# Kernel optimization log

Measured on AMD Instinct MI355X. Metric: run time of the kernel, lower is better.

The kernel has to match this reference:

```python
import jax, jax.numpy as jnp
from jax import lax
import numpy as np

N_VOX = 50000
B = 2
D, H, W = 8, 160, 160
CIN = 16
G = 3
K = 27
CHANS = [(16, 16), (16, 32), (32, 64), (64, 64), (64, 128)]
NAMES = ['in', 'e1', 'e2', 'e3', 'out']


def setup_inputs() -> dict:
    key = jax.random.key(0)
    ks = jax.random.split(key, 16)
    rng = np.random.default_rng(0)
    # unique active cells -> deterministic scatter/gather rulebook
    lin = rng.choice(B * D * H * W, size=N_VOX, replace=False)
    bz = lin // (D * H * W)
    rem = lin % (D * H * W)
    zz = rem // (H * W)
    yy = (rem % (H * W)) // W
    xx = rem % W
    coors = jnp.asarray(np.stack([bz, zz, yy, xx], 1).astype(np.int32))
    inp = {
        'voxel_features': jax.random.normal(ks[0], (N_VOX, CIN), jnp.float32),
        'coors': coors,
        'batch_size': B,
    }
    i = 1
    for nm, (ci, co) in zip(NAMES, CHANS):
        k1, k2 = jax.random.split(ks[i]); i += 1
        inp['wb_' + nm] = jax.random.normal(k1, (K, ci, co), jnp.float32) * 0.05
        inp['ws_' + nm] = jax.random.normal(k2, (K, ci, G, co), jnp.float32) * 0.05
        inp['gm_' + nm] = jnp.ones((co,), jnp.float32)
        inp['bt_' + nm] = jnp.zeros((co,), jnp.float32)
    return inp


def _kan_block(feat, nbr, wb, ws, gm, bt, centers, inv_h):
    # submanifold KAN conv: gather -> (silu base + RBF spline basis) GEMM -> accumulate
    n = feat.shape[0]
    fp = jnp.concatenate([feat, jnp.zeros((1, feat.shape[1]), feat.dtype)], 0)  # pad row for out-of-grid

    def body(acc, kin):
        idx, wbk, wsk = kin
        x = fp[idx]                                   # [N, Cin] gathered neighbors
        base = jax.nn.silu(x) @ wbk                   # [N, Cout]
        bas = jnp.exp(-jnp.square((x[:, :, None] - centers) * inv_h))  # [N, Cin, G]
        spl = jnp.einsum('ncg,cgo->no', bas, wsk)     # [N, Cout]
        return acc + base + spl, None

    out0 = jnp.zeros((n, wb.shape[-1]), feat.dtype)
    out, _ = lax.scan(jax.checkpoint(body), out0, (nbr, wb, ws))
    # BatchNorm1d (train-mode batch stats) + ReLU
    mu = out.mean(0)
    var = out.var(0)
    out = (out - mu) * lax.rsqrt(var + 1e-3) * gm + bt
    return jax.nn.relu(out)


def _build_rulebook(coors, batch_size, n):
    grid = jnp.full((batch_size, D + 2, H + 2, W + 2), n, jnp.int32)
    grid = grid.at[coors[:, 0], coors[:, 1] + 1, coors[:, 2] + 1, coors[:, 3] + 1].set(
        jnp.arange(n, dtype=jnp.int32))
    offs = [(dz, dy, dx) for dz in (-1, 0, 1) for dy in (-1, 0, 1) for dx in (-1, 0, 1)]
    return jnp.stack([
        grid[coors[:, 0], coors[:, 1] + 1 + dz, coors[:, 2] + 1 + dy, coors[:, 3] + 1 + dx]
        for dz, dy, dx in offs])  # [27, N]


def reference(voxel_features, coors, batch_size,
              wb_in, ws_in, gm_in, bt_in,
              wb_e1, ws_e1, gm_e1, bt_e1,
              wb_e2, ws_e2, gm_e2, bt_e2,
              wb_e3, ws_e3, gm_e3, bt_e3,
              wb_out, ws_out, gm_out, bt_out):
    n = voxel_features.shape[0]
    nbr = _build_rulebook(coors, batch_size, n)
    centers = jnp.linspace(-1.0, 1.0, G)
    inv_h = (G - 1) / 2.0
    x = _kan_block(voxel_features, nbr, wb_in, ws_in, gm_in, bt_in, centers, inv_h)
    x = _kan_block(x, nbr, wb_e1, ws_e1, gm_e1, bt_e1, centers, inv_h)
    x = _kan_block(x, nbr, wb_e2, ws_e2, gm_e2, bt_e2, centers, inv_h)
    x = _kan_block(x, nbr, wb_e3, ws_e3, gm_e3, bt_e3, centers, inv_h)
    x = _kan_block(x, nbr, wb_out, ws_out, gm_out, bt_out, centers, inv_h)
    co = x.shape[1]
    dense = jnp.zeros((batch_size, D, H, W, co), x.dtype)
    dense = dense.at[coors[:, 0], coors[:, 1], coors[:, 2], coors[:, 3]].set(x)
    dense = dense.transpose(0, 4, 1, 2, 3)            # [B, C, D, H, W]
    return dense.reshape(batch_size, co * D, H, W)    # [B, C*D, H, W]
```

## Files before the change

### kernel.cpp

```cpp
#include <hip/hip_runtime.h>

#define N_VOX 50000
#define BATCH 2
#define DD 8
#define HH 160
#define WW 160
#define PD 10
#define PH 162
#define PW 162
#define KK 27
#define NCELL (BATCH*DD*HH*WW)
#define GRID_ELEMS (BATCH*PD*PH*PW)
#define OUT_ELEMS (BATCH*128*DD*HH*WW)

typedef __attribute__((ext_vector_type(8))) short short8v;
typedef __attribute__((ext_vector_type(4))) float float4v;

__device__ inline unsigned short f2bf(float f) {
    unsigned u = __float_as_uint(f);
    u += 0x7FFFu + ((u >> 16) & 1u);
    return (unsigned short)(u >> 16);
}

__device__ inline void gload_lds16(const void* g, void* l) {
    __builtin_amdgcn_global_load_lds(
        (const __attribute__((address_space(1))) void*)g,
        (__attribute__((address_space(3))) void*)l, 16, 0, 0);
}

__global__ void k_flags(const int* __restrict__ coors, int* __restrict__ flags) {
    int n = blockIdx.x * 256 + threadIdx.x;
    if (n >= N_VOX) return;
    int b = coors[n*4+0], z = coors[n*4+1], y = coors[n*4+2], x = coors[n*4+3];
    flags[((b*DD + z)*HH + y)*WW + x] = 1;
}

__global__ void k_scan1(const int* __restrict__ flags, int* __restrict__ scanout,
                        int* __restrict__ bsums) {
    __shared__ int s[256];
    int t = threadIdx.x, blk = blockIdx.x;
    int4 v = ((const int4*)(flags + blk*1024))[t];
    int tsum = v.x + v.y + v.z + v.w;
    s[t] = tsum; __syncthreads();
    for (int off = 1; off < 256; off <<= 1) {
        int x = (t >= off) ? s[t-off] : 0;
        __syncthreads(); s[t] += x; __syncthreads();
    }
    int excl = s[t] - tsum;
    int4 o; o.x = excl; o.y = excl + v.x; o.z = o.y + v.y; o.w = o.z + v.z;
    ((int4*)(scanout + blk*1024))[t] = o;
    if (t == 255) bsums[blk] = s[255];
}

__global__ void k_scan2(int* __restrict__ bsums) {
    __shared__ int s[512];
    int t = threadIdx.x;
    int orig = (t < 400) ? bsums[t] : 0;
    s[t] = orig; __syncthreads();
    for (int off = 1; off < 512; off <<= 1) {
        int x = (t >= off) ? s[t-off] : 0;
        __syncthreads(); s[t] += x; __syncthreads();
    }
    if (t < 400) bsums[t] = s[t] - orig;
}

__global__ void k_pos(const int* __restrict__ coors, const int* __restrict__ scanout,
                      const int* __restrict__ bsums, int* __restrict__ pos_of,
                      int* __restrict__ vox_at) {
    int n = blockIdx.x * 256 + threadIdx.x;
    if (n >= N_VOX) return;
    int b = coors[n*4+0], z = coors[n*4+1], y = coors[n*4+2], x = coors[n*4+3];
    int lin = ((b*DD + z)*HH + y)*WW + x;
    int pos = scanout[lin] + bsums[lin >> 10];
    pos_of[n] = pos;
    vox_at[pos] = n;
}

__global__ void k_gridP(const int* __restrict__ coors, const int* __restrict__ pos_of,
                        int* __restrict__ gridP) {
    int n = blockIdx.x * 256 + threadIdx.x;
    if (n >= N_VOX) return;
    int b = coors[n*4+0], z = coors[n*4+1], y = coors[n*4+2], x = coors[n*4+3];
    gridP[((b*PD + z+1)*PH + (y+1))*PW + (x+1)] = pos_of[n];
}

__global__ void k_nbrP(const int* __restrict__ coors, const int* __restrict__ vox_at,
                       const int* __restrict__ gridP, int* __restrict__ nbrP) {
    int i = blockIdx.x * 256 + threadIdx.x;
    if (i >= N_VOX) return;
    int n = vox_at[i];
    int b = coors[n*4+0], z = coors[n*4+1]+1, y = coors[n*4+2]+1, x = coors[n*4+3]+1;
    int k = 0;
    for (int dz = -1; dz <= 1; ++dz)
        for (int dy = -1; dy <= 1; ++dy)
            for (int dx = -1; dx <= 1; ++dx) {
                int g = gridP[((b*PD + z+dz)*PH + (y+dy))*PW + (x+dx)];
                nbrP[k*N_VOX + i] = (g >= 0) ? g : N_VOX;
                ++k;
            }
}

__global__ void k_phi0(const float* __restrict__ vf, const int* __restrict__ vox_at,
                       unsigned short* __restrict__ phi) {
    int e = blockIdx.x * 256 + threadIdx.x;
    if (e >= (N_VOX + 1) * 16) return;
    int i = e / 16, c = e % 16;
    float x = 0.f;
    if (i < N_VOX) x = vf[(size_t)vox_at[i] * 16 + c];
    float sig = 1.f / (1.f + __expf(-x));
    ushort4 p;
    p.x = f2bf(x * sig);
    p.y = f2bf(__expf(-(x + 1.f) * (x + 1.f)));
    p.z = f2bf(__expf(-x * x));
    p.w = f2bf(__expf(-(x - 1.f) * (x - 1.f)));
    *(ushort4*)&phi[(size_t)e * 4] = p;
}

struct WswzArgs {
    const float* wb[5];
    const float* ws[5];
    unsigned short* dst[5];
};
__global__ void k_wswz_all(WswzArgs a) {
    constexpr int off[6]   = {0, 27648, 82944, 304128, 746496, 1631232};
    constexpr int lgCI4[5] = {6, 6, 7, 8, 8};
    constexpr int lgCO[5]  = {4, 5, 6, 6, 7};
    int e = blockIdx.x * 256 + threadIdx.x;
    if (e >= off[5]) return;
    int L = 0;
    #pragma unroll
    for (int i = 1; i < 5; ++i) L += (e >= off[i]);
    int el = e - off[L];
    int CIN4 = 1 << lgCI4[L], COUT = 1 << lgCO[L], CIN = CIN4 >> 2;
    int j8   = el & 7;
    int rest = el >> 3;
    int o    = rest & (COUT - 1);
    int kb   = rest >> lgCO[L];
    int kabs = kb * 8 + j8;
    int k  = kabs >> lgCI4[L];
    int c4 = kabs & (CIN4 - 1);
    int c = c4 >> 2, jj = c4 & 3;
    float v = (jj == 0) ? a.wb[L][(k * CIN + c) * COUT + o]
                        : a.ws[L][((k * CIN + c) * 3 + (jj - 1)) * COUT + o];
    a.dst[L][el] = f2bf(v);
}

template<int CIN, int COUT, int NSPL>
__global__ __launch_bounds__(64, 2) void k_conv_mfma(
    const unsigned short* __restrict__ phi,
    const int*            __restrict__ nbrP,
    const unsigned short* __restrict__ Wsw,
    float*                __restrict__ pre,
    float*                __restrict__ sums)
{
    constexpr int CIN4   = CIN * 4;
    constexpr int BK     = 64;
    constexpr int SPK    = CIN4 / BK;
    constexpr int NSTAGE = KK * SPK;
    constexpr int COUTH  = COUT / NSPL;
    constexpr int NFW    = COUTH / 16;
    constexpr int WR     = 4;
    constexpr int NMB    = (N_VOX + 63) / 64;
    constexpr int NBLK   = NMB * NSPL;
    constexpr int PERX   = (NBLK + 7) / 8;

    int lb = blockIdx.x;
    int linear = (lb & 7) * PERX + (lb >> 3);
    if (linear >= NBLK) return;
    const int mb = linear / NSPL, h = linear % NSPL;

    const int lane = threadIdx.x & 63;
    const int l15 = lane & 15, q = lane >> 4;
    const int base = mb * 64;
    int vg[WR];
    #pragma unroll
    for (int rs = 0; rs < WR; ++rs) vg[rs] = base + rs * 16 + l15;
    const int ob = h * COUTH;

    const unsigned short* bp = Wsw + (size_t)(q * COUT + ob + l15) * 8;

    int rows[WR], rowsN[WR];
    short8v A0[2][WR], A1[2][WR];
    short8v B0[2][NFW], B1[2][NFW];

    auto loadB = [&](int sp, short8v (&Bb)[2][NFW]) {
        #pragma unroll
        for (int kk = 0; kk < 2; ++kk)
            #pragma unroll
            for (int nf = 0; nf < NFW; ++nf)
                Bb[kk][nf] = *(const short8v*)(bp +
                    ((size_t)(sp * 8 + kk * 4) * COUT + nf * 16) * 8);
    };
    auto loadA = [&](int sp, short8v (&Ab)[2][WR]) {
        if (sp % SPK == 0) {
            #pragma unroll
            for (int rs = 0; rs < WR; ++rs) rows[rs] = rowsN[rs];
        }
        const int c4s = (sp % SPK) * BK;
        #pragma unroll
        for (int rs = 0; rs < WR; ++rs) {
            const unsigned short* p = phi + (size_t)rows[rs] * CIN4 + c4s + q * 8;
            Ab[0][rs] = *(const short8v*)p;
            Ab[1][rs] = *(const short8v*)(p + 32);
        }
        if (sp % SPK == 0) {
            int k2 = sp / SPK + 1;
            if (k2 < KK) {
                #pragma unroll
                for (int rs = 0; rs < WR; ++rs)
                    rowsN[rs] = (vg[rs] < N_VOX) ? nbrP[k2 * N_VOX + vg[rs]] : N_VOX;
            }
        }
    };

    float4v acc[WR][NFW];
    #pragma unroll
    for (int rs = 0; rs < WR; ++rs)
        #pragma unroll
        for (int nf = 0; nf < NFW; ++nf)
            acc[rs][nf] = (float4v){0.f, 0.f, 0.f, 0.f};

    auto domfma = [&](const short8v (&Ab)[2][WR], const short8v (&Bb)[2][NFW]) {
        #pragma unroll
        for (int kk = 0; kk < 2; ++kk)
            #pragma unroll
            for (int nf = 0; nf < NFW; ++nf)
                #pragma unroll
                for (int rs = 0; rs < WR; ++rs)
                    acc[rs][nf] = __builtin_amdgcn_mfma_f32_16x16x32_bf16(
                        Ab[kk][rs], Bb[kk][nf], acc[rs][nf], 0, 0, 0);
    };

    #pragma unroll
    for (int rs = 0; rs < WR; ++rs) {
        rows[rs]  = (vg[rs] < N_VOX) ? nbrP[vg[rs]] : N_VOX;
        rowsN[rs] = (vg[rs] < N_VOX) ? nbrP[N_VOX + vg[rs]] : N_VOX;
    }
    loadB(0, B0);
    #pragma unroll
    for (int rs = 0; rs < WR; ++rs) {
        const unsigned short* p = phi + (size_t)rows[rs] * CIN4 + q * 8;
        A0[0][rs] = *(const short8v*)p;
        A0[1][rs] = *(const short8v*)(p + 32);
    }

    #define SLOT(T, Ac, Bc, An, Bn)                                   \
        if ((T) + 1 < NSTAGE) { loadB((T) + 1, Bn); loadA((T) + 1, An); } \
        __builtin_amdgcn_sched_barrier(0);                            \
        domfma(Ac, Bc);

    int s = 0;
    for (; s + 2 <= NSTAGE; s += 2) {
        SLOT(s + 0, A0, B0, A1, B1)
        SLOT(s + 1, A1, B1, A0, B0)
    }
    if constexpr (NSTAGE % 2 != 0) {
        domfma(A0, B0);
    }
    #undef SLOT

    #pragma unroll
    for (int rs = 0; rs < WR; ++rs)
        #pragma unroll
        for (int nf = 0; nf < NFW; ++nf)
            #pragma unroll
            for (int r = 0; r < 4; ++r) {
                int v = base + rs * 16 + q * 4 + r;
                if (v < N_VOX)
                    pre[(size_t)v * COUT + ob + nf * 16 + l15] = acc[rs][nf][r];
            }

    float* S = sums + (blockIdx.x & 7) * 256;
    #pragma unroll
    for (int nf = 0; nf < NFW; ++nf) {
        float s1 = 0.f, s2 = 0.f;
        #pragma unroll
        for (int rs = 0; rs < WR; ++rs)
            #pragma unroll
            for (int r = 0; r < 4; ++r) {
                int v = base + rs * 16 + q * 4 + r;
                if (v < N_VOX) {
                    float a = acc[rs][nf][r];
                    s1 += a; s2 += a * a;
                }
            }
        s1 += __shfl_xor(s1, 16); s1 += __shfl_xor(s1, 32);
        s2 += __shfl_xor(s2, 16); s2 += __shfl_xor(s2, 32);
        if (q == 0) {
            atomicAdd(&S[ob + nf * 16 + l15], s1);
            atomicAdd(&S[COUT + ob + nf * 16 + l15], s2);
        }
    }
}

template<int CIN, int COUT>
__global__ __launch_bounds__(256, 2) void k_conv_lds(
    const unsigned short* __restrict__ phi,
    const int*            __restrict__ nbrP,
    const unsigned short* __restrict__ Wsw,
    float*                __restrict__ pre,
    float*                __restrict__ sums)
{
    constexpr int CIN4   = CIN * 4;
    constexpr int BK     = 64;
    constexpr int SPK    = CIN4 / BK;
    constexpr int NSTAGE = KK * SPK;
    constexpr int NFW    = COUT / 32;
    constexpr int NMB    = (N_VOX + 127) / 128;
    constexpr int PERX   = (NMB + 7) / 8;
    constexpr int BENT   = 8 * COUT;
    constexpr int NBI    = (BENT / 64) / 4;

    __shared__ short8v lds[2 * 1024 + 2 * BENT];

    int lb = blockIdx.x;
    int mb = (lb & 7) * PERX + (lb >> 3);
    if (mb >= NMB) return;

    const int t = threadIdx.x, lane = t & 63, w = t >> 6;
    const int l15 = lane & 15, q = lane >> 4;
    const int wm = w >> 1, wn = w & 1;
    const int base = mb * 128;
    const int ob = wn * (COUT / 2);

    short8v* ldsA = lds;
    short8v* ldsB = lds + 2048;

    auto nbrR = [&](int k, int j) -> int {
        return (base + j < N_VOX) ? nbrP[k * N_VOX + base + j] : N_VOX;
    };
    int r0 = nbrR(0, lane), r1 = nbrR(0, 64 + lane);
    int rn0 = nbrR(1, lane), rn1 = nbrR(1, 64 + lane);

    auto stage = [&](int spn) {
        const int nb = spn & 1;
        const int cs = (spn % SPK) * BK;
        #pragma unroll
        for (int i = 0; i < 4; ++i) {
            const int m = w * 4 + i;
            const int c = m >> 1, half = m & 1;
            const unsigned short* src =
                phi + (size_t)(half ? r1 : r0) * CIN4 + cs + c * 8;
            gload_lds16(src, ldsA + nb * 1024 + m * 64);
        }
        #pragma unroll
        for (int i = 0; i < NBI; ++i) {
            const int m = w * NBI + i;
            const unsigned short* src =
                Wsw + ((size_t)spn * BENT + m * 64 + lane) * 8;
            gload_lds16(src, ldsB + nb * BENT + m * 64);
        }
    };

    float4v acc[4][NFW];
    #pragma unroll
    for (int rs = 0; rs < 4; ++rs)
        #pragma unroll
        for (int nf = 0; nf < NFW; ++nf)
            acc[rs][nf] = (float4v){0.f, 0.f, 0.f, 0.f};

    stage(0);
    asm volatile("s_waitcnt vmcnt(0)" ::: "memory");
    __builtin_amdgcn_sched_barrier(0);
    __builtin_amdgcn_s_barrier();
    __builtin_amdgcn_sched_barrier(0);

    for (int sp = 0; sp < NSTAGE; ++sp) {
        const int spn = sp + 1;
        if (spn < NSTAGE) {
            if (spn % SPK == 0) {
                r0 = rn0; r1 = rn1;
                int k2 = spn / SPK + 1;
                if (k2 < KK) { rn0 = nbrR(k2, lane); rn1 = nbrR(k2, 64 + lane); }
            }
            stage(spn);
        }
        __builtin_amdgcn_sched_barrier(0);
        const short8v* A = ldsA + (sp & 1) * 1024 + wm * 64 + l15;
        const short8v* B = ldsB + (sp & 1) * BENT + ob + l15;
        short8v af[2][4], bf[2][NFW];
        #pragma unroll
        for (int kk = 0; kk < 2; ++kk) {
            #pragma unroll
            for (int rs = 0; rs < 4; ++rs)
                af[kk][rs] = A[(kk * 4 + q) * 128 + rs * 16];
            #pragma unroll
            for (int nf = 0; nf < NFW; ++nf)
                bf[kk][nf] = B[(kk * 4 + q) * COUT + nf * 16];
        }
        #pragma unroll
        for (int kk = 0; kk < 2; ++kk)
            #pragma unroll
            for (int nf = 0; nf < NFW; ++nf)
                #pragma unroll
                for (int rs = 0; rs < 4; ++rs)
                    acc[rs][nf] = __builtin_amdgcn_mfma_f32_16x16x32_bf16(
                        af[kk][rs], bf[kk][nf], acc[rs][nf], 0, 0, 0);
        if (spn < NSTAGE) {
            asm volatile("s_waitcnt vmcnt(0)" ::: "memory");
            __builtin_amdgcn_sched_barrier(0);
            __builtin_amdgcn_s_barrier();
            __builtin_amdgcn_sched_barrier(0);
        }
    }

    #pragma unroll
    for (int rs = 0; rs < 4; ++rs)
        #pragma unroll
        for (int nf = 0; nf < NFW; ++nf)
            #pragma unroll
            for (int r = 0; r < 4; ++r) {
                int v = base + wm * 64 + rs * 16 + q * 4 + r;
                if (v < N_VOX)
                    pre[(size_t)v * COUT + ob + nf * 16 + l15] = acc[rs][nf][r];
            }

    float* S = sums + (blockIdx.x & 7) * 256;
    #pragma unroll
    for (int nf = 0; nf < NFW; ++nf) {
        float s1 = 0.f, s2 = 0.f;
        #pragma unroll
        for (int rs = 0; rs < 4; ++rs)
            #pragma unroll
            for (int r = 0; r < 4; ++r) {
                int v = base + wm * 64 + rs * 16 + q * 4 + r;
                if (v < N_VOX) {
                    float a = acc[rs][nf][r];
                    s1 += a; s2 += a * a;
                }
            }
        s1 += __shfl_xor(s1, 16); s1 += __shfl_xor(s1, 32);
        s2 += __shfl_xor(s2, 16); s2 += __shfl_xor(s2, 32);
        if (q == 0) {
            atomicAdd(&S[ob + nf * 16 + l15], s1);
            atomicAdd(&S[COUT + ob + nf * 16 + l15], s2);
        }
    }
}

template<int COUT>
__global__ void k_bnapply_phi(const float* __restrict__ pre, const float* __restrict__ sums,
                              const float* __restrict__ gm, const float* __restrict__ bt,
                              unsigned short* __restrict__ phi) {
    __shared__ float sc[COUT], sh[COUT];
    int t = threadIdx.x;
    if (t < COUT) {
        float s1 = 0.f, s2 = 0.f;
        #pragma unroll
        for (int xo = 0; xo < 8; ++xo) {
            s1 += sums[xo * 256 + t];
            s2 += sums[xo * 256 + COUT + t];
        }
        float mu  = s1 * (1.f / N_VOX);
        float var = s2 * (1.f / N_VOX) - mu*mu;
        float s = rsqrtf(var + 1e-3f) * gm[t];
        sc[t] = s;
        sh[t] = bt[t] - mu * s;
    }
    __syncthreads();
    int tot = (N_VOX + 1) * COUT;
    for (int e = blockIdx.x*256 + t; e < tot; e += gridDim.x*256) {
        int i = e / COUT, c = e % COUT;
        float x = 0.f;
        if (i < N_VOX) x = fmaxf(pre[(size_t)i*COUT + c] * sc[c] + sh[c], 0.f);
        float sig = 1.f / (1.f + __expf(-x));
        ushort4 p;
        p.x = f2bf(x * sig);
        p.y = f2bf(__expf(-(x + 1.f) * (x + 1.f)));
        p.z = f2bf(__expf(-x * x));
        p.w = f2bf(__expf(-(x - 1.f) * (x - 1.f)));
        *(ushort4*)&phi[(size_t)e * 4] = p;
    }
}

template<int COUT>
__global__ void k_bnapply_f32(float* __restrict__ pre, const float* __restrict__ sums,
                              const float* __restrict__ gm, const float* __restrict__ bt) {
    __shared__ float sc[COUT], sh[COUT];
    int t = threadIdx.x;
    if (t < COUT) {
        float s1 = 0.f, s2 = 0.f;
        #pragma unroll
        for (int xo = 0; xo < 8; ++xo) {
            s1 += sums[xo * 256 + t];
            s2 += sums[xo * 256 + COUT + t];
        }
        float mu  = s1 * (1.f / N_VOX);
        float var = s2 * (1.f / N_VOX) - mu*mu;
        float s = rsqrtf(var + 1e-3f) * gm[t];
        sc[t] = s;
        sh[t] = bt[t] - mu * s;
    }
    __syncthreads();
    for (int e = blockIdx.x*256 + t; e < N_VOX*COUT; e += gridDim.x*256) {
        int c = e % COUT;
        pre[e] = fmaxf(pre[e] * sc[c] + sh[c], 0.f);
    }
}

__global__ void k_dense(const float* __restrict__ feat, const int* __restrict__ gridP,
                        float* __restrict__ out) {
    int e4 = blockIdx.x*256 + threadIdx.x;
    if (e4 >= OUT_ELEMS/4) return;
    int e = e4 * 4;
    int x  = e % WW;
    int y  = (e / WW) % HH;
    int cz = (e / (WW*HH)) % (128*DD);
    int b  = e / (WW*HH*128*DD);
    int c = cz >> 3, z = cz & 7;
    const int* gp = &gridP[((b*PD + z+1)*PH + (y+1))*PW + (x+1)];
    int g0 = gp[0], g1 = gp[1], g2 = gp[2], g3 = gp[3];
    float4 o;
    o.x = (g0 >= 0) ? feat[(size_t)g0*128 + c] : 0.f;
    o.y = (g1 >= 0) ? feat[(size_t)g1*128 + c] : 0.f;
    o.z = (g2 >= 0) ? feat[(size_t)g2*128 + c] : 0.f;
    o.w = (g3 >= 0) ? feat[(size_t)g3*128 + c] : 0.f;
    *(float4*)&out[e] = o;
}

template<int CIN, int COUT, int NSPL>
static void run_block(const float* gm, const float* bt,
                      const int* nbrP, unsigned short* phi, const unsigned short* Wsw,
                      float* sums, float* pre, bool last, hipStream_t stream) {
    constexpr int NMB  = (N_VOX + 63) / 64;
    constexpr int NBLK = NMB * NSPL;
    constexpr int GRID = ((NBLK + 7) / 8) * 8;
    k_conv_mfma<CIN, COUT, NSPL><<<GRID, 64, 0, stream>>>(phi, nbrP, Wsw, pre, sums);
    if (last) {
        k_bnapply_f32<COUT><<<512, 256, 0, stream>>>(pre, sums, gm, bt);
    } else {
        k_bnapply_phi<COUT><<<512, 256, 0, stream>>>(pre, sums, gm, bt, phi);
    }
}

template<int CIN, int COUT>
static void run_block_lds(const float* gm, const float* bt,
                          const int* nbrP, unsigned short* phi, const unsigned short* Wsw,
                          float* sums, float* pre, bool last, hipStream_t stream) {
    constexpr int NMB  = (N_VOX + 127) / 128;
    constexpr int GRID = ((NMB + 7) / 8) * 8;
    k_conv_lds<CIN, COUT><<<GRID, 256, 0, stream>>>(phi, nbrP, Wsw, pre, sums);
    if (last) {
        k_bnapply_f32<COUT><<<512, 256, 0, stream>>>(pre, sums, gm, bt);
    } else {
        k_bnapply_phi<COUT><<<512, 256, 0, stream>>>(pre, sums, gm, bt, phi);
    }
}

extern "C" void kernel_launch(void* const* d_in, const int* in_sizes, int n_in,
                              void* d_out, int out_size, void* d_ws, size_t ws_size,
                              hipStream_t stream) {
    const float* vf    = (const float*)d_in[0];
    const int*   coors = (const int*)d_in[1];
    const float* wb[5] = {(const float*)d_in[3],  (const float*)d_in[7],
                          (const float*)d_in[11], (const float*)d_in[15],
                          (const float*)d_in[19]};
    const float* wsp[5]= {(const float*)d_in[4],  (const float*)d_in[8],
                          (const float*)d_in[12], (const float*)d_in[16],
                          (const float*)d_in[20]};
    const float* gm[5] = {(const float*)d_in[5],  (const float*)d_in[9],
                          (const float*)d_in[13], (const float*)d_in[17],
                          (const float*)d_in[21]};
    const float* bt[5] = {(const float*)d_in[6],  (const float*)d_in[10],
                          (const float*)d_in[14], (const float*)d_in[18],
                          (const float*)d_in[22]};

    char* p = (char*)d_ws;
    auto alloc = [&](size_t bytes) {
        char* r = p;
        p += (bytes + 255) & ~(size_t)255;
        return r;
    };
    int*            flags   = (int*)           alloc((size_t)NCELL * 4);
    int*            scanout = (int*)           alloc((size_t)NCELL * 4);
    int*            bsums   = (int*)           alloc(512 * 4);
    int*            pos_of  = (int*)           alloc((size_t)N_VOX * 4);
    int*            vox_at  = (int*)           alloc((size_t)N_VOX * 4);
    int*            gridP   = (int*)           alloc((size_t)GRID_ELEMS * 4);
    int*            nbrP    = (int*)           alloc((size_t)KK * N_VOX * 4);
    unsigned short* Wsw0    = (unsigned short*)alloc((size_t)KK * 64  * 16  * 2);
    unsigned short* Wsw1    = (unsigned short*)alloc((size_t)KK * 64  * 32  * 2);
    unsigned short* Wsw2    = (unsigned short*)alloc((size_t)KK * 128 * 64  * 2);
    unsigned short* Wsw3    = (unsigned short*)alloc((size_t)KK * 256 * 64  * 2);
    unsigned short* Wsw4    = (unsigned short*)alloc((size_t)KK * 256 * 128 * 2);
    unsigned short* phi     = (unsigned short*)alloc((size_t)(N_VOX + 1) * 256 * 2);
    float*          sumsAll = (float*)         alloc(5 * 8 * 256 * 4);
    float*          pre     = (float*)         alloc((size_t)N_VOX * 128 * 4);

    hipMemsetAsync(flags, 0, (size_t)NCELL * 4, stream);
    hipMemsetAsync(gridP, 0xFF, (size_t)GRID_ELEMS * 4, stream);
    hipMemsetAsync(sumsAll, 0, 5 * 8 * 256 * 4, stream);

    WswzArgs wa;
    for (int i = 0; i < 5; ++i) { wa.wb[i] = wb[i]; wa.ws[i] = wsp[i]; }
    wa.dst[0] = Wsw0; wa.dst[1] = Wsw1; wa.dst[2] = Wsw2; wa.dst[3] = Wsw3; wa.dst[4] = Wsw4;
    k_wswz_all<<<(1631232 + 255) / 256, 256, 0, stream>>>(wa);

    k_flags<<<(N_VOX+255)/256, 256, 0, stream>>>(coors, flags);
    k_scan1<<<NCELL/1024, 256, 0, stream>>>(flags, scanout, bsums);
    k_scan2<<<1, 512, 0, stream>>>(bsums);
    k_pos  <<<(N_VOX+255)/256, 256, 0, stream>>>(coors, scanout, bsums, pos_of, vox_at);
    k_gridP<<<(N_VOX+255)/256, 256, 0, stream>>>(coors, pos_of, gridP);
    k_nbrP <<<(N_VOX+255)/256, 256, 0, stream>>>(coors, vox_at, gridP, nbrP);
    {
        int n = (N_VOX + 1) * 16;
        k_phi0<<<(n + 255) / 256, 256, 0, stream>>>(vf, vox_at, phi);
    }

    run_block<16, 16, 1>(gm[0], bt[0], nbrP, phi, Wsw0, sumsAll + 0*2048, pre, false, stream);
    run_block<16, 32, 1>(gm[1], bt[1], nbrP, phi, Wsw1, sumsAll + 1*2048, pre, false, stream);
    run_block_lds<32, 64 >(gm[2], bt[2], nbrP, phi, Wsw2, sumsAll + 2*2048, pre, false, stream);
    run_block_lds<64, 64 >(gm[3], bt[3], nbrP, phi, Wsw3, sumsAll + 3*2048, pre, false, stream);
    run_block_lds<64, 128>(gm[4], bt[4], nbrP, phi, Wsw4, sumsAll + 4*2048, pre, true,  stream);

    k_dense<<<(OUT_ELEMS/4 + 255)/256, 256, 0, stream>>>(pre, gridP, (float*)d_out);
}
```

Measured before the change: 661.8 us.

## Share weight tiles in LDS per offset, load gathered activations directly to registers

The 256-thread conv kernel for the later blocks is replaced by one that keeps only the weight tile in LDS. The weights for a whole kernel offset are double-buffered there, and each wave gathers its own 32 voxel rows straight into registers, software-pipelined one sub-stage ahead. The last block also splits its output channels across two blocks. This removes the activation LDS staging and cuts the per-substage barriers to one per offset, at the cost of more uncoalesced direct global gathers and a duplicated activation read in the split layer.

Result: faster. 633.5 us (-4.3%).

```diff
diff --git a/kernel.cpp b/kernel.cpp
--- a/kernel.cpp
+++ b/kernel.cpp
@@ -293,8 +293,8 @@
     }
 }
 
-template<int CIN, int COUT>
-__global__ __launch_bounds__(256, 2) void k_conv_lds(
+template<int CIN, int COUT, int NSPL>
+__global__ __launch_bounds__(256, 2) void k_conv_bsh(
     const unsigned short* __restrict__ phi,
     const int*            __restrict__ nbrP,
     const unsigned short* __restrict__ Wsw,
@@ -305,112 +305,126 @@
     constexpr int BK     = 64;
     constexpr int SPK    = CIN4 / BK;
     constexpr int NSTAGE = KK * SPK;
-    constexpr int NFW    = COUT / 32;
+    constexpr int KB_G   = 8 * SPK;
+    constexpr int COUTH  = COUT / NSPL;
+    constexpr int NFW    = COUTH / 16;
+    constexpr int WR     = 2;
     constexpr int NMB    = (N_VOX + 127) / 128;
-    constexpr int PERX   = (NMB + 7) / 8;
-    constexpr int BENT   = 8 * COUT;
-    constexpr int NBI    = (BENT / 64) / 4;
-
-    __shared__ short8v lds[2 * 1024 + 2 * BENT];
+    constexpr int NBLK   = NMB * NSPL;
+    constexpr int PERX   = (NBLK + 7) / 8;
+    constexpr int SI     = 2 * SPK;
+    constexpr int VMCG   = 4 * SPK + 2;
+
+    __shared__ short8v ldsB[2][KB_G][64];
 
     int lb = blockIdx.x;
-    int mb = (lb & 7) * PERX + (lb >> 3);
-    if (mb >= NMB) return;
+    int linear = (lb & 7) * PERX + (lb >> 3);
+    if (linear >= NBLK) return;
+    const int mb = linear / NSPL, h = linear % NSPL;
 
     const int t = threadIdx.x, lane = t & 63, w = t >> 6;
     const int l15 = lane & 15, q = lane >> 4;
-    const int wm = w >> 1, wn = w & 1;
-    const int base = mb * 128;
-    const int ob = wn * (COUT / 2);
-
-    short8v* ldsA = lds;
-    short8v* ldsB = lds + 2048;
-
-    auto nbrR = [&](int k, int j) -> int {
-        return (base + j < N_VOX) ? nbrP[k * N_VOX + base + j] : N_VOX;
+    const int base = mb * 128 + w * 32;
+    int vg[WR];
+    #pragma unroll
+    for (int rs = 0; rs < WR; ++rs) vg[rs] = base + rs * 16 + l15;
+    const int ob = h * COUTH;
+
+    int rows[WR], rowsN[WR];
+    short8v A0[2][WR], A1[2][WR];
+
+    auto stage = [&](int g) {
+        #pragma unroll
+        for (int j = 0; j < SI; ++j) {
+            const int m = w * SI + j;
+            gload_lds16(Wsw + ((size_t)(g * KB_G + m) * COUT + ob + lane) * 8,
+                        &ldsB[g & 1][m][0]);
+        }
     };
-    int r0 = nbrR(0, lane), r1 = nbrR(0, 64 + lane);
-    int rn0 = nbrR(1, lane), rn1 = nbrR(1, 64 + lane);
-
-    auto stage = [&](int spn) {
-        const int nb = spn & 1;
-        const int cs = (spn % SPK) * BK;
-        #pragma unroll
-        for (int i = 0; i < 4; ++i) {
-            const int m = w * 4 + i;
-            const int c = m >> 1, half = m & 1;
-            const unsigned short* src =
-                phi + (size_t)(half ? r1 : r0) * CIN4 + cs + c * 8;
-            gload_lds16(src, ldsA + nb * 1024 + m * 64);
-        }
-        #pragma unroll
-        for (int i = 0; i < NBI; ++i) {
-            const int m = w * NBI + i;
-            const unsigned short* src =
-                Wsw + ((size_t)spn * BENT + m * 64 + lane) * 8;
-            gload_lds16(src, ldsB + nb * BENT + m * 64);
+    auto loadA = [&](int sp, short8v (&Ab)[2][WR]) {
+        if (sp % SPK == 0) {
+            #pragma unroll
+            for (int rs = 0; rs < WR; ++rs) rows[rs] = rowsN[rs];
+        }
+        const int c4s = (sp % SPK) * BK;
+        #pragma unroll
+        for (int rs = 0; rs < WR; ++rs) {
+            const unsigned short* p = phi + (size_t)rows[rs] * CIN4 + c4s + q * 8;
+            Ab[0][rs] = *(const short8v*)p;
+            Ab[1][rs] = *(const short8v*)(p + 32);
+        }
+        if (sp % SPK == 0) {
+            int k2 = sp / SPK + 1;
+            if (k2 < KK) {
+                #pragma unroll
+                for (int rs = 0; rs < WR; ++rs)
+                    rowsN[rs] = (vg[rs] < N_VOX) ? nbrP[k2 * N_VOX + vg[rs]] : N_VOX;
+            }
         }
     };
 
-    float4v acc[4][NFW];
-    #pragma unroll
-    for (int rs = 0; rs < 4; ++rs)
+    float4v acc[WR][NFW];
+    #pragma unroll
+    for (int rs = 0; rs < WR; ++rs)
         #pragma unroll
         for (int nf = 0; nf < NFW; ++nf)
             acc[rs][nf] = (float4v){0.f, 0.f, 0.f, 0.f};
 
     stage(0);
-    asm volatile("s_waitcnt vmcnt(0)" ::: "memory");
     __builtin_amdgcn_sched_barrier(0);
-    __builtin_amdgcn_s_barrier();
-    __builtin_amdgcn_sched_barrier(0);
-
-    for (int sp = 0; sp < NSTAGE; ++sp) {
-        const int spn = sp + 1;
-        if (spn < NSTAGE) {
-            if (spn % SPK == 0) {
-                r0 = rn0; r1 = rn1;
-                int k2 = spn / SPK + 1;
-                if (k2 < KK) { rn0 = nbrR(k2, lane); rn1 = nbrR(k2, 64 + lane); }
-            }
-            stage(spn);
-        }
+    #pragma unroll
+    for (int rs = 0; rs < WR; ++rs) {
+        rows[rs]  = (vg[rs] < N_VOX) ? nbrP[vg[rs]] : N_VOX;
+        rowsN[rs] = (vg[rs] < N_VOX) ? nbrP[N_VOX + vg[rs]] : N_VOX;
+    }
+    #pragma unroll
+    for (int rs = 0; rs < WR; ++rs) {
+        const unsigned short* p = phi + (size_t)rows[rs] * CIN4 + q * 8;
+        A0[0][rs] = *(const short8v*)p;
+        A0[1][rs] = *(const short8v*)(p + 32);
+    }
+
+    int sp = 0;
+    #define SLOTB(SG, Ac, An)                                                 \
+    {                                                                         \
+        short8v bf[2][NFW];                                                   \
+        _Pragma("unroll") for (int kk = 0; kk < 2; ++kk)                      \
+        _Pragma("unroll") for (int nf = 0; nf < NFW; ++nf)                    \
+            bf[kk][nf] = ldsB[g & 1][(SG) * 8 + kk * 4 + q][nf * 16 + l15];   \
+        if (sp + 1 < NSTAGE) loadA(sp + 1, An);                               \
+        __builtin_amdgcn_sched_barrier(0);                                    \
+        _Pragma("unroll") for (int kk = 0; kk < 2; ++kk)                      \
+        _Pragma("unroll") for (int nf = 0; nf < NFW; ++nf)                    \
+        _Pragma("unroll") for (int rs = 0; rs < WR; ++rs)                     \
+            acc[rs][nf] = __builtin_amdgcn_mfma_f32_16x16x32_bf16(            \
+                Ac[kk][rs], bf[kk][nf], acc[rs][nf], 0, 0, 0);                \
+        ++sp;                                                                 \
+    }
+
+    for (int g = 0; g < KK; ++g) {
+        if (g == 0) { asm volatile("s_waitcnt vmcnt(8)" ::: "memory"); }
+        else        { asm volatile("s_waitcnt vmcnt(%0)" :: "i"(VMCG) : "memory"); }
         __builtin_amdgcn_sched_barrier(0);
-        const short8v* A = ldsA + (sp & 1) * 1024 + wm * 64 + l15;
-        const short8v* B = ldsB + (sp & 1) * BENT + ob + l15;
-        short8v af[2][4], bf[2][NFW];
-        #pragma unroll
-        for (int kk = 0; kk < 2; ++kk) {
-            #pragma unroll
-            for (int rs = 0; rs < 4; ++rs)
-                af[kk][rs] = A[(kk * 4 + q) * 128 + rs * 16];
-            #pragma unroll
-            for (int nf = 0; nf < NFW; ++nf)
-                bf[kk][nf] = B[(kk * 4 + q) * COUT + nf * 16];
-        }
-        #pragma unroll
-        for (int kk = 0; kk < 2; ++kk)
-            #pragma unroll
-            for (int nf = 0; nf < NFW; ++nf)
-                #pragma unroll
-                for (int rs = 0; rs < 4; ++rs)
-                    acc[rs][nf] = __builtin_amdgcn_mfma_f32_16x16x32_bf16(
-                        af[kk][rs], bf[kk][nf], acc[rs][nf], 0, 0, 0);
-        if (spn < NSTAGE) {
-            asm volatile("s_waitcnt vmcnt(0)" ::: "memory");
-            __builtin_amdgcn_sched_barrier(0);
-            __builtin_amdgcn_s_barrier();
-            __builtin_amdgcn_sched_barrier(0);
-        }
-    }
-
-    #pragma unroll
-    for (int rs = 0; rs < 4; ++rs)
+        __builtin_amdgcn_s_barrier();
+        __builtin_amdgcn_sched_barrier(0);
+        if (g + 1 < KK) stage(g + 1);
+        __builtin_amdgcn_sched_barrier(0);
+        SLOTB(0, A0, A1)
+        SLOTB(1, A1, A0)
+        if constexpr (SPK == 4) {
+            SLOTB(2, A0, A1)
+            SLOTB(3, A1, A0)
+        }
+    }
+    #undef SLOTB
+
+    #pragma unroll
+    for (int rs = 0; rs < WR; ++rs)
         #pragma unroll
         for (int nf = 0; nf < NFW; ++nf)
             #pragma unroll
             for (int r = 0; r < 4; ++r) {
-                int v = base + wm * 64 + rs * 16 + q * 4 + r;
+                int v = base + rs * 16 + q * 4 + r;
                 if (v < N_VOX)
                     pre[(size_t)v * COUT + ob + nf * 16 + l15] = acc[rs][nf][r];
             }
@@ -420,10 +434,10 @@
     for (int nf = 0; nf < NFW; ++nf) {
         float s1 = 0.f, s2 = 0.f;
         #pragma unroll
-        for (int rs = 0; rs < 4; ++rs)
+        for (int rs = 0; rs < WR; ++rs)
             #pragma unroll
             for (int r = 0; r < 4; ++r) {
-                int v = base + wm * 64 + rs * 16 + q * 4 + r;
+                int v = base + rs * 16 + q * 4 + r;
                 if (v < N_VOX) {
                     float a = acc[rs][nf][r];
                     s1 += a; s2 += a * a;
@@ -533,13 +547,14 @@
     }
 }
 
-template<int CIN, int COUT>
-static void run_block_lds(const float* gm, const float* bt,
+template<int CIN, int COUT, int NSPL>
+static void run_block_bsh(const float* gm, const float* bt,
                           const int* nbrP, unsigned short* phi, const unsigned short* Wsw,
                           float* sums, float* pre, bool last, hipStream_t stream) {
     constexpr int NMB  = (N_VOX + 127) / 128;
-    constexpr int GRID = ((NMB + 7) / 8) * 8;
-    k_conv_lds<CIN, COUT><<<GRID, 256, 0, stream>>>(phi, nbrP, Wsw, pre, sums);
+    constexpr int NBLK = NMB * NSPL;
+    constexpr int GRID = ((NBLK + 7) / 8) * 8;
+    k_conv_bsh<CIN, COUT, NSPL><<<GRID, 256, 0, stream>>>(phi, nbrP, Wsw, pre, sums);
     if (last) {
         k_bnapply_f32<COUT><<<512, 256, 0, stream>>>(pre, sums, gm, bt);
     } else {
@@ -609,9 +624,9 @@
 
     run_block<16, 16, 1>(gm[0], bt[0], nbrP, phi, Wsw0, sumsAll + 0*2048, pre, false, stream);
     run_block<16, 32, 1>(gm[1], bt[1], nbrP, phi, Wsw1, sumsAll + 1*2048, pre, false, stream);
-    run_block_lds<32, 64 >(gm[2], bt[2], nbrP, phi, Wsw2, sumsAll + 2*2048, pre, false, stream);
-    run_block_lds<64, 64 >(gm[3], bt[3], nbrP, phi, Wsw3, sumsAll + 3*2048, pre, false, stream);
-    run_block_lds<64, 128>(gm[4], bt[4], nbrP, phi, Wsw4, sumsAll + 4*2048, pre, true,  stream);
+    run_block_bsh<32, 64,  1>(gm[2], bt[2], nbrP, phi, Wsw2, sumsAll + 2*2048, pre, false, stream);
+    run_block_bsh<64, 64,  1>(gm[3], bt[3], nbrP, phi, Wsw3, sumsAll + 3*2048, pre, false, stream);
+    run_block_bsh<64, 128, 2>(gm[4], bt[4], nbrP, phi, Wsw4, sumsAll + 4*2048, pre, true,  stream);
 
     k_dense<<<(OUT_ELEMS/4 + 255)/256, 256, 0, stream>>>(pre, gridP, (float*)d_out);
 }
```
